# Kernel optimization log

Measured on AMD Instinct MI355X. Metric: run time of the kernel, lower is better.

Reference implementation:

```python
import jax, jax.numpy as jnp
import numpy as np

B, S, IN_DIM, D, H, L = 2, 2048, 64, 512, 8, 2
DK = D // H
EPS = 1e-5

def _layernorm(x, g, b):
    mu = jnp.mean(x, axis=-1, keepdims=True)
    var = jnp.mean((x - mu) ** 2, axis=-1, keepdims=True)
    return (x - mu) * jax.lax.rsqrt(var + EPS) * g + b

def _prob_sparse_layer(x, Wq, bq, Wk, bk, Wv, bv, fcW, fcb, ln_g, ln_b):
    # x: [B, S, D]
    Bs, Ss, _ = x.shape
    Q = (x @ Wq + bq).reshape(Bs, Ss, H, DK).transpose(0, 2, 1, 3)  # [B,H,S,DK]
    K = (x @ Wk + bk).reshape(Bs, Ss, H, DK).transpose(0, 2, 1, 3)
    V = (x @ Wv + bv).reshape(Bs, Ss, H, DK).transpose(0, 2, 1, 3)
    scores = jnp.einsum('bhqd,bhkd->bhqk', Q, K) / np.sqrt(DK).astype(np.float32)
    k = max(1, Ss // 10)
    top_scores, _ = jax.lax.top_k(scores, k)          # [B,H,S,k]
    threshold = top_scores[..., -1:]                  # k-th largest per row
    sparse_scores = jnp.where(scores < threshold, -jnp.inf, scores)
    attn = jax.nn.softmax(sparse_scores, axis=-1)     # dropout is identity in eval
    out = jnp.einsum('bhqk,bhkd->bhqd', attn, V)
    out = out.transpose(0, 2, 1, 3).reshape(Bs, Ss, D)
    out = out @ fcW + fcb
    return _layernorm(x + out, ln_g, ln_b)

def setup_inputs() -> dict:
    key = jax.random.key(0)
    ks = jax.random.split(key, 16)
    sd = 1.0 / np.sqrt(D)
    sdi = 1.0 / np.sqrt(IN_DIM)
    return {
        'x': jax.random.normal(ks[0], (B, S, IN_DIM), jnp.float32),
        'enc_W': jax.random.normal(ks[1], (IN_DIM, D), jnp.float32) * sdi,
        'enc_b': jnp.zeros((D,), jnp.float32),
        'Wq': jax.random.normal(ks[2], (L, D, D), jnp.float32) * sd,
        'bq': jnp.zeros((L, D), jnp.float32),
        'Wk': jax.random.normal(ks[3], (L, D, D), jnp.float32) * sd,
        'bk': jnp.zeros((L, D), jnp.float32),
        'Wv': jax.random.normal(ks[4], (L, D, D), jnp.float32) * sd,
        'bv': jnp.zeros((L, D), jnp.float32),
        'fcW': jax.random.normal(ks[5], (L, D, D), jnp.float32) * sd,
        'fcb': jnp.zeros((L, D), jnp.float32),
        'ln_g': jnp.ones((L, D), jnp.float32),
        'ln_b': jnp.zeros((L, D), jnp.float32),
        'dec_W': jax.random.normal(ks[6], (D, IN_DIM), jnp.float32) * sd,
        'dec_b': jnp.zeros((IN_DIM,), jnp.float32),
    }

def reference(x, enc_W, enc_b, Wq, bq, Wk, bk, Wv, bv, fcW, fcb, ln_g, ln_b, dec_W, dec_b):
    h = x @ enc_W + enc_b  # [B,S,D]
    for i in range(Wq.shape[0]):
        h = _prob_sparse_layer(h, Wq[i], bq[i], Wk[i], bk[i], Wv[i], bv[i],
                               fcW[i], fcb[i], ln_g[i], ln_b[i])
    return h[:, -1, :] @ dec_W + dec_b  # [B, IN_DIM]
```

## Files before the change

kernel.cpp:

```cpp
#include <hip/hip_runtime.h>
#include <hip/hip_bf16.h>

typedef unsigned short u16;
typedef __bf16 bf16x8 __attribute__((ext_vector_type(8)));
typedef u16 u16x8 __attribute__((ext_vector_type(8)));
typedef float f32x4 __attribute__((ext_vector_type(4)));

#define S_LEN 2048
#define NH 8
#define DMODEL 512
#define TOPK 204

__device__ __forceinline__ u16 f2b(float f) {
  __hip_bfloat16 h = __float2bfloat16(f);
  return __builtin_bit_cast(u16, h);
}
__device__ __forceinline__ unsigned f2b_fast(float f) {
  unsigned u = __float_as_uint(f);
  return (u + 0x7FFFu + ((u >> 16) & 1u)) >> 16;
}
__device__ __forceinline__ float kunmap(unsigned k) {
  unsigned tb = (k & 0x8000u) ? (k ^ 0x8000u) : (~k & 0xFFFFu);
  return __uint_as_float(tb << 16);
}
__device__ __forceinline__ unsigned fkmap(float f) {
  unsigned b = __float_as_uint(f) >> 16;
  return b ^ ((b & 0x8000u) ? 0xFFFFu : 0x8000u);
}

__global__ void transpose_w(const float* __restrict__ in, u16* __restrict__ out, int R, int C) {
  __shared__ float tile[32][33];
  int c0 = blockIdx.x * 32, r0 = blockIdx.y * 32;
  int tx = threadIdx.x & 31, ty = threadIdx.x >> 5;
#pragma unroll
  for (int i = 0; i < 32; i += 8)
    tile[ty + i][tx] = in[(long long)(r0 + ty + i) * C + c0 + tx];
  __syncthreads();
#pragma unroll
  for (int i = 0; i < 32; i += 8)
    out[(long long)(c0 + ty + i) * R + r0 + tx] = f2b(tile[tx][ty + i]);
}

__global__ void transpose_w4(const float* __restrict__ W0, const float* __restrict__ W1,
                             const float* __restrict__ W2, const float* __restrict__ W3,
                             u16* __restrict__ O0, u16* __restrict__ O1,
                             u16* __restrict__ O2, u16* __restrict__ O3) {
  __shared__ float tile[32][33];
  const float* in;
  u16* out;
  switch (blockIdx.z) {
    case 0: in = W0; out = O0; break;
    case 1: in = W1; out = O1; break;
    case 2: in = W2; out = O2; break;
    default: in = W3; out = O3; break;
  }
  int c0 = blockIdx.x * 32, r0 = blockIdx.y * 32;
  int tx = threadIdx.x & 31, ty = threadIdx.x >> 5;
#pragma unroll
  for (int i = 0; i < 32; i += 8)
    tile[ty + i][tx] = in[(long long)(r0 + ty + i) * 512 + c0 + tx];
  __syncthreads();
#pragma unroll
  for (int i = 0; i < 32; i += 8)
    out[(long long)(c0 + ty + i) * 512 + r0 + tx] = f2b(tile[tx][ty + i]);
}

__global__ void conv_b(const float* __restrict__ in, u16* __restrict__ out, int n) {
  int i = blockIdx.x * 256 + threadIdx.x;
  if (i < n) out[i] = f2b(in[i]);
}

template <int MODE>
__global__ __launch_bounds__(256) void gemm_bt(
    const u16* __restrict__ A, const u16* __restrict__ BT,
    const float* __restrict__ bias, const float* __restrict__ biasK, const float* __restrict__ biasV,
    float* __restrict__ outF, u16* __restrict__ outB, u16* __restrict__ outBK, u16* __restrict__ outBV,
    int M, int N, int K, float scale) {
  __shared__ u16 As[64 * 32];
  __shared__ u16 Bs[128 * 32];
  int n0 = blockIdx.x * 128, m0 = blockIdx.y * 64;
  int t = threadIdx.x;
  int lane = t & 63, wv = t >> 6;
  int mw = (wv & 1) * 32, nw = (wv >> 1) * 64;
  int fr = lane & 15, fg = lane >> 4;
  f32x4 acc[2][4] = {};
  for (int kt = 0; kt < K; kt += 32) {
    int e0 = t * 8;
    int r0r = e0 >> 5, c0c = e0 & 31;
    int e1 = e0 + 2048;
    int r1r = e1 >> 5, c1c = e1 & 31;
    *(u16x8*)&As[e0] = *(const u16x8*)&A[(long long)(m0 + r0r) * K + kt + c0c];
    *(u16x8*)&Bs[e0] = *(const u16x8*)&BT[(long long)(n0 + r0r) * K + kt + c0c];
    *(u16x8*)&Bs[e1] = *(const u16x8*)&BT[(long long)(n0 + r1r) * K + kt + c1c];
    __syncthreads();
    bf16x8 af[2], bfv[4];
#pragma unroll
    for (int i = 0; i < 2; i++) af[i] = *(const bf16x8*)&As[(mw + i * 16 + fr) * 32 + fg * 8];
#pragma unroll
    for (int j = 0; j < 4; j++) bfv[j] = *(const bf16x8*)&Bs[(nw + j * 16 + fr) * 32 + fg * 8];
#pragma unroll
    for (int i = 0; i < 2; i++)
#pragma unroll
      for (int j = 0; j < 4; j++)
        acc[i][j] = __builtin_amdgcn_mfma_f32_16x16x32_bf16(af[i], bfv[j], acc[i][j], 0, 0, 0);
    __syncthreads();
  }
#pragma unroll
  for (int i = 0; i < 2; i++)
#pragma unroll
    for (int j = 0; j < 4; j++) {
      int mloc = mw + i * 16 + fg * 4;
      int n = n0 + nw + j * 16 + fr;
      float bvl;
      if constexpr (MODE == 5) {
        int seg = n >> 9, nn = n & 511;
        bvl = (seg == 0 ? bias : seg == 1 ? biasK : biasV)[nn];
      } else {
        bvl = bias ? bias[n] : 0.f;
      }
#pragma unroll
      for (int r = 0; r < 4; r++) {
        int m = m0 + mloc + r;
        float v = acc[i][j][r] * scale + bvl;
        if constexpr (MODE == 0) {
          outF[(long long)m * N + n] = v;
        } else if constexpr (MODE == 4) {
          outF[(long long)m * N + n] = v;
          outB[(long long)m * N + n] = f2b(v);
        } else if constexpr (MODE == 5) {
          int seg = n >> 9, nn = n & 511;
          if (seg == 0) v *= 0.125f;
          u16 val = f2b(v);
          if (seg == 2) {
            outBV[((long long)((m >> 11) * NH + (nn >> 6)) * 64 + (nn & 63)) * S_LEN + (m & 2047)] = val;
          } else {
            long long qkidx = (long long)((m >> 11) * NH + (nn >> 6)) * (S_LEN * 64) +
                              (long long)(m & 2047) * 64 + (nn & 63);
            if (seg == 0) outB[qkidx] = val;
            else outBK[qkidx] = val;
          }
        }
      }
    }
}

__global__ __launch_bounds__(1024, 8) void score_pv(
    const u16* __restrict__ Qb, const u16* __restrict__ Kb, const u16* __restrict__ VTb,
    u16* __restrict__ aoB) {
  __shared__ u16 Qs[16 * 64];
  __shared__ __align__(16) u16 Ss[16 * 2048];
  __shared__ float thrS[16];
  __shared__ float mS[16];
  __shared__ float zS[16 * 16];
  int flat = blockIdx.x;
  int xcd = flat & 7, local = flat >> 3;
  int bh = xcd * 2 + (local >> 7);
  int m0 = (local & 127) * 16;
  int t = threadIdx.x;
  int lane = t & 63, wv = t >> 6, fr = lane & 15, fg = lane >> 4;
  const u16* Qg = Qb + ((long long)bh * S_LEN + m0) * 64;
  const u16* Kg = Kb + (long long)bh * S_LEN * 64;
  const u16* Vg = VTb + (long long)bh * 64 * S_LEN;
  if (t < 128) {
    int row = t >> 3, cc = t & 7;
    *(u16x8*)&Qs[row * 64 + ((cc ^ (row & 7)) * 8)] = *(const u16x8*)&Qg[row * 64 + cc * 8];
  }
  __syncthreads();
  bf16x8 aq[2];
#pragma unroll
  for (int ks = 0; ks < 2; ks++)
    aq[ks] = *(const bf16x8*)&Qs[fr * 64 + (((fg + 4 * ks) ^ (fr & 7)) * 8)];

#pragma unroll 4
  for (int tt = 0; tt < 8; tt++) {
    int col0 = wv * 128 + tt * 16;
    f32x4 acc = {};
#pragma unroll
    for (int ks = 0; ks < 2; ks++) {
      bf16x8 bk = *(const bf16x8*)&Kg[(long long)(col0 + fr) * 64 + ks * 32 + fg * 8];
      acc = __builtin_amdgcn_mfma_f32_16x16x32_bf16(bk, aq[ks], acc, 0, 0, 0);
    }
    uint2 w;
    w.x = f2b_fast(acc[0]) | (f2b_fast(acc[1]) << 16);
    w.y = f2b_fast(acc[2]) | (f2b_fast(acc[3]) << 16);
    int row = fr, col = col0 + fg * 4;
    *(uint2*)&Ss[row * 2048 + (col ^ ((row & 15) << 3))] = w;
  }
  __syncthreads();

  {
    int rr = wv;
    const uint2* cu2 = (const uint2*)&Ss[rr * 2048];
    float kf[32];
#pragma unroll
    for (int j = 0; j < 8; j++) {
      uint2 w = cu2[lane + 64 * j];
      kf[4 * j + 0] = __uint_as_float(w.x << 16);
      kf[4 * j + 1] = __uint_as_float(w.x & 0xFFFF0000u);
      kf[4 * j + 2] = __uint_as_float(w.y << 16);
      kf[4 * j + 3] = __uint_as_float(w.y & 0xFFFF0000u);
    }
    float mxf = kf[0];
#pragma unroll
    for (int j = 1; j < 32; j++) mxf = fmaxf(mxf, kf[j]);
#pragma unroll
    for (int o = 1; o < 64; o <<= 1)
      mxf = fmaxf(mxf, __uint_as_float((unsigned)__shfl_xor((int)__float_as_uint(mxf), o)));
    unsigned mxi = fkmap(mxf);
    unsigned lo, hi;
    unsigned lo0 = mxi > 384u ? mxi - 384u : 0u;
    {
      float pf = kunmap(lo0);
      int c = 0;
#pragma unroll
      for (int j = 0; j < 32; j++) c += (int)__popcll(__ballot(kf[j] >= pf));
      if (c >= TOPK) { lo = lo0; hi = mxi; }
      else { lo = 0u; hi = lo0 - 1u; }
    }
    while (lo < hi) {
      unsigned mid = (lo + hi + 1u) >> 1;
      float midf = kunmap(mid);
      int c = 0;
#pragma unroll
      for (int j = 0; j < 32; j++) c += (int)__popcll(__ballot(kf[j] >= midf));
      if (c >= TOPK) lo = mid; else hi = mid - 1u;
    }
    if (lane == 0) {
      thrS[rr] = kunmap(lo);
      mS[rr] = mxf;
    }
  }
  __syncthreads();

  float thrF = thrS[fr];
  float myM = mS[fr];
  float zpart = 0.f;
  f32x4 acc_o[4] = {};
#pragma unroll 2
  for (int step = 0; step < 4; step++) {
    int k0 = wv * 128 + step * 32;
    u16x8 kk = *(const u16x8*)&Ss[fr * 2048 + ((k0 + fg * 8) ^ ((fr & 15) << 3))];
    unsigned wp[4];
#pragma unroll
    for (int e2 = 0; e2 < 4; e2++) {
      float s0 = __uint_as_float((unsigned)kk[2 * e2] << 16);
      float s1 = __uint_as_float((unsigned)kk[2 * e2 + 1] << 16);
      float p0 = (s0 >= thrF) ? __expf(s0 - myM) : 0.f;
      float p1 = (s1 >= thrF) ? __expf(s1 - myM) : 0.f;
      zpart += p0 + p1;
      wp[e2] = f2b_fast(p0) | (f2b_fast(p1) << 16);
    }
    bf16x8 pa = *(bf16x8*)&wp;
#pragma unroll
    for (int j = 0; j < 4; j++) {
      bf16x8 bv = *(const bf16x8*)&Vg[(long long)(j * 16 + fr) * 2048 + k0 + fg * 8];
      acc_o[j] = __builtin_amdgcn_mfma_f32_16x16x32_bf16(pa, bv, acc_o[j], 0, 0, 0);
    }
  }
  zpart += __shfl_xor(zpart, 16);
  zpart += __shfl_xor(zpart, 32);
  __syncthreads();

  float* Of = (float*)Ss;
#pragma unroll
  for (int j = 0; j < 4; j++)
#pragma unroll
    for (int r = 0; r < 4; r++) {
      int row = fg * 4 + r, col = j * 16 + fr;
      Of[wv * 1024 + row * 64 + (col ^ ((row >> 2) << 3))] = acc_o[j][r];
    }
  if (fg == 0) zS[wv * 16 + fr] = zpart;
  __syncthreads();
  long long ob = (long long)(bh >> 3) * S_LEN * DMODEL + (bh & 7) * 64;
  {
    int row = t >> 6, dk = t & 63;
    int sw = dk ^ ((row >> 2) << 3);
    float s = 0.f;
#pragma unroll
    for (int w = 0; w < 16; w++) s += Of[w * 1024 + row * 64 + sw];
    float z = 0.f;
#pragma unroll
    for (int w = 0; w < 16; w++) z += zS[w * 16 + row];
    aoB[ob + (long long)(m0 + row) * DMODEL + dk] = f2b(s / z);
  }
}

__global__ __launch_bounds__(256) void resid_ln(const float* __restrict__ h, const float* __restrict__ fco,
                                                const float* __restrict__ g, const float* __restrict__ b,
                                                float* __restrict__ hout, u16* __restrict__ hbout) {
  __shared__ float red[4];
  int row = blockIdx.x;
  int t = threadIdx.x;
  long long base = (long long)row * 512;
  float v0 = h[base + t] + fco[base + t];
  float v1 = h[base + t + 256] + fco[base + t + 256];
  float s = v0 + v1;
#pragma unroll
  for (int o = 32; o > 0; o >>= 1) s += __shfl_down(s, o);
  if ((t & 63) == 0) red[t >> 6] = s;
  __syncthreads();
  float mu = (red[0] + red[1] + red[2] + red[3]) * (1.f / 512.f);
  float d0 = v0 - mu, d1 = v1 - mu;
  float q = d0 * d0 + d1 * d1;
#pragma unroll
  for (int o = 32; o > 0; o >>= 1) q += __shfl_down(q, o);
  __syncthreads();
  if ((t & 63) == 0) red[t >> 6] = q;
  __syncthreads();
  float var = (red[0] + red[1] + red[2] + red[3]) * (1.f / 512.f);
  float rs = rsqrtf(var + 1e-5f);
  float y0 = d0 * rs * g[t] + b[t];
  float y1 = d1 * rs * g[t + 256] + b[t + 256];
  hout[base + t] = y0;
  hout[base + t + 256] = y1;
  hbout[base + t] = f2b(y0);
  hbout[base + t + 256] = f2b(y1);
}

__global__ void decoder_k(const float* __restrict__ h, const float* __restrict__ W,
                          const float* __restrict__ bias, float* __restrict__ out) {
  int t = threadIdx.x;
  int b = t >> 6, j = t & 63;
  const float* hr = h + ((long long)b * S_LEN + (S_LEN - 1)) * DMODEL;
  float s = 0.f;
  for (int d = 0; d < DMODEL; d++) s += hr[d] * W[(long long)d * 64 + j];
  out[t] = s + bias[j];
}

extern "C" void kernel_launch(void* const* d_in, const int* in_sizes, int n_in,
                              void* d_out, int out_size, void* d_ws, size_t ws_size,
                              hipStream_t stream) {
  const float* x = (const float*)d_in[0];
  const float* enc_W = (const float*)d_in[1];
  const float* enc_b = (const float*)d_in[2];
  const float* Wq = (const float*)d_in[3];
  const float* bq = (const float*)d_in[4];
  const float* Wk = (const float*)d_in[5];
  const float* bk = (const float*)d_in[6];
  const float* Wv = (const float*)d_in[7];
  const float* bv = (const float*)d_in[8];
  const float* fcW = (const float*)d_in[9];
  const float* fcb = (const float*)d_in[10];
  const float* ln_g = (const float*)d_in[11];
  const float* ln_b = (const float*)d_in[12];
  const float* dec_W = (const float*)d_in[13];
  const float* dec_b = (const float*)d_in[14];

  char* p = (char*)d_ws;
  auto alloc = [&](size_t bytes) {
    char* r = p;
    p += (bytes + 255) & ~(size_t)255;
    return r;
  };
  const size_t BS = 2 * (size_t)S_LEN;
  u16* encWT = (u16*)alloc(512 * 64 * 2);
  u16* xbf = (u16*)alloc(BS * 64 * 2);
  float* hF = (float*)alloc(BS * 512 * 4);
  u16* hB = (u16*)alloc(BS * 512 * 2);
  u16* WqT = (u16*)alloc(512 * 512 * 2);
  u16* WkT = (u16*)alloc(512 * 512 * 2);
  u16* WvT = (u16*)alloc(512 * 512 * 2);
  u16* fcWT = (u16*)alloc(512 * 512 * 2);
  u16* Qb = (u16*)alloc((size_t)16 * 2048 * 64 * 2);
  u16* Kb = (u16*)alloc((size_t)16 * 2048 * 64 * 2);
  u16* VTb = (u16*)alloc((size_t)16 * 2048 * 64 * 2);
  u16* aoB = (u16*)alloc(BS * 512 * 2);
  float* fcO = (float*)Qb;

  transpose_w<<<dim3(16, 2), 256, 0, stream>>>(enc_W, encWT, 64, 512);
  conv_b<<<(int)(BS * 64 / 256), 256, 0, stream>>>(x, xbf, (int)(BS * 64));
  gemm_bt<4><<<dim3(4, 64), 256, 0, stream>>>(xbf, encWT, enc_b, nullptr, nullptr,
                                              hF, hB, nullptr, nullptr, 4096, 512, 64, 1.f);

  for (int l = 0; l < 2; l++) {
    transpose_w4<<<dim3(16, 16, 4), 256, 0, stream>>>(
        Wq + (size_t)l * 512 * 512, Wk + (size_t)l * 512 * 512,
        Wv + (size_t)l * 512 * 512, fcW + (size_t)l * 512 * 512,
        WqT, WkT, WvT, fcWT);
    gemm_bt<5><<<dim3(12, 64), 256, 0, stream>>>(hB, WqT, bq + l * 512, bk + l * 512, bv + l * 512,
                                                 nullptr, Qb, Kb, VTb, 4096, 1536, 512, 1.f);
    score_pv<<<dim3(2048), 1024, 0, stream>>>(Qb, Kb, VTb, aoB);
    gemm_bt<0><<<dim3(4, 64), 256, 0, stream>>>(aoB, fcWT, fcb + l * 512, nullptr, nullptr,
                                                fcO, nullptr, nullptr, nullptr, 4096, 512, 512, 1.f);
    resid_ln<<<4096, 256, 0, stream>>>(hF, fcO, ln_g + l * 512, ln_b + l * 512, hF, hB);
  }
  decoder_k<<<1, 128, 0, stream>>>(hF, dec_W, dec_b, (float*)d_out);
}
```

Measured before the change: 391.9 us.

## Fuse row max into score pass, prefetch K/V, vectorize reductions, split decoder

Computes the per-row score maximum during the QK^T MFMA pass via shuffles and an LDS atomicMax, removing a separate max reduction before the top-k threshold search. K and V fragments are software-prefetched one iteration ahead, and bf16 conversions are replaced with truncation. The output reduction is rewritten to use vectorized f32x4 LDS stores and loads with a precomputed reciprocal normalizer. The decoder is parallelized across more threads and blocks. Truncation slightly changes rounding of scores and probabilities, and the lower occupancy hint may affect register allocation.

```diff
diff --git a/kernel.cpp b/kernel.cpp
--- a/kernel.cpp
+++ b/kernel.cpp
@@ -15,15 +15,11 @@
   __hip_bfloat16 h = __float2bfloat16(f);
   return __builtin_bit_cast(u16, h);
 }
-__device__ __forceinline__ unsigned f2b_fast(float f) {
-  unsigned u = __float_as_uint(f);
-  return (u + 0x7FFFu + ((u >> 16) & 1u)) >> 16;
-}
 __device__ __forceinline__ float kunmap(unsigned k) {
   unsigned tb = (k & 0x8000u) ? (k ^ 0x8000u) : (~k & 0xFFFFu);
   return __uint_as_float(tb << 16);
 }
-__device__ __forceinline__ unsigned fkmap(float f) {
+__device__ __forceinline__ unsigned fkmap_t(float f) {
   unsigned b = __float_as_uint(f) >> 16;
   return b ^ ((b & 0x8000u) ? 0xFFFFu : 0x8000u);
 }
@@ -144,14 +140,16 @@
     }
 }
 
-__global__ __launch_bounds__(1024, 8) void score_pv(
+__global__ __launch_bounds__(1024, 4) void score_pv(
     const u16* __restrict__ Qb, const u16* __restrict__ Kb, const u16* __restrict__ VTb,
     u16* __restrict__ aoB) {
   __shared__ u16 Qs[16 * 64];
   __shared__ __align__(16) u16 Ss[16 * 2048];
+  __shared__ unsigned maxkS[16];
   __shared__ float thrS[16];
   __shared__ float mS[16];
   __shared__ float zS[16 * 16];
+  __shared__ float rzS[16];
   int flat = blockIdx.x;
   int xcd = flat & 7, local = flat >> 3;
   int bh = xcd * 2 + (local >> 7);
@@ -161,6 +159,7 @@
   const u16* Qg = Qb + ((long long)bh * S_LEN + m0) * 64;
   const u16* Kg = Kb + (long long)bh * S_LEN * 64;
   const u16* Vg = VTb + (long long)bh * 64 * S_LEN;
+  if (t < 16) maxkS[t] = 0u;
   if (t < 128) {
     int row = t >> 3, cc = t & 7;
     *(u16x8*)&Qs[row * 64 + ((cc ^ (row & 7)) * 8)] = *(const u16x8*)&Qg[row * 64 + cc * 8];
@@ -171,51 +170,65 @@
   for (int ks = 0; ks < 2; ks++)
     aq[ks] = *(const bf16x8*)&Qs[fr * 64 + (((fg + 4 * ks) ^ (fr & 7)) * 8)];
 
-#pragma unroll 4
+  float rowmax = -3e38f;
+  int colb = wv * 128;
+  bf16x8 ka = *(const bf16x8*)&Kg[(long long)(colb + fr) * 64 + fg * 8];
+  bf16x8 kb = *(const bf16x8*)&Kg[(long long)(colb + fr) * 64 + 32 + fg * 8];
+#pragma unroll
   for (int tt = 0; tt < 8; tt++) {
-    int col0 = wv * 128 + tt * 16;
+    bf16x8 na = ka, nb = kb;
+    if (tt < 7) {
+      int c2 = colb + (tt + 1) * 16;
+      na = *(const bf16x8*)&Kg[(long long)(c2 + fr) * 64 + fg * 8];
+      nb = *(const bf16x8*)&Kg[(long long)(c2 + fr) * 64 + 32 + fg * 8];
+    }
     f32x4 acc = {};
-#pragma unroll
-    for (int ks = 0; ks < 2; ks++) {
-      bf16x8 bk = *(const bf16x8*)&Kg[(long long)(col0 + fr) * 64 + ks * 32 + fg * 8];
-      acc = __builtin_amdgcn_mfma_f32_16x16x32_bf16(bk, aq[ks], acc, 0, 0, 0);
-    }
+    acc = __builtin_amdgcn_mfma_f32_16x16x32_bf16(ka, aq[0], acc, 0, 0, 0);
+    acc = __builtin_amdgcn_mfma_f32_16x16x32_bf16(kb, aq[1], acc, 0, 0, 0);
+    rowmax = fmaxf(fmaxf(acc[0], acc[1]), fmaxf(rowmax, fmaxf(acc[2], acc[3])));
+    unsigned u0 = __float_as_uint(acc[0]), u1 = __float_as_uint(acc[1]);
+    unsigned u2 = __float_as_uint(acc[2]), u3 = __float_as_uint(acc[3]);
     uint2 w;
-    w.x = f2b_fast(acc[0]) | (f2b_fast(acc[1]) << 16);
-    w.y = f2b_fast(acc[2]) | (f2b_fast(acc[3]) << 16);
-    int row = fr, col = col0 + fg * 4;
-    *(uint2*)&Ss[row * 2048 + (col ^ ((row & 15) << 3))] = w;
-  }
+    w.x = (u0 >> 16) | (u1 & 0xFFFF0000u);
+    w.y = (u2 >> 16) | (u3 & 0xFFFF0000u);
+    int col = colb + tt * 16 + fg * 4;
+    *(uint2*)&Ss[fr * 2048 + (col ^ ((fr & 15) << 3))] = w;
+    ka = na;
+    kb = nb;
+  }
+  rowmax = fmaxf(rowmax, __uint_as_float((unsigned)__shfl_xor((int)__float_as_uint(rowmax), 16)));
+  rowmax = fmaxf(rowmax, __uint_as_float((unsigned)__shfl_xor((int)__float_as_uint(rowmax), 32)));
+  if (fg == 0) atomicMax(&maxkS[fr], fkmap_t(rowmax));
   __syncthreads();
 
   {
     int rr = wv;
-    const uint2* cu2 = (const uint2*)&Ss[rr * 2048];
+    unsigned mxi = __builtin_amdgcn_readfirstlane(maxkS[rr]);
+    unsigned swz = (unsigned)((rr & 15) << 3);
     float kf[32];
 #pragma unroll
-    for (int j = 0; j < 8; j++) {
-      uint2 w = cu2[lane + 64 * j];
-      kf[4 * j + 0] = __uint_as_float(w.x << 16);
-      kf[4 * j + 1] = __uint_as_float(w.x & 0xFFFF0000u);
-      kf[4 * j + 2] = __uint_as_float(w.y << 16);
-      kf[4 * j + 3] = __uint_as_float(w.y & 0xFFFF0000u);
-    }
-    float mxf = kf[0];
-#pragma unroll
-    for (int j = 1; j < 32; j++) mxf = fmaxf(mxf, kf[j]);
-#pragma unroll
-    for (int o = 1; o < 64; o <<= 1)
-      mxf = fmaxf(mxf, __uint_as_float((unsigned)__shfl_xor((int)__float_as_uint(mxf), o)));
-    unsigned mxi = fkmap(mxf);
+    for (int j2 = 0; j2 < 4; j2++) {
+      uint4 q = *(const uint4*)&Ss[rr * 2048 + (((unsigned)(lane * 8 + j2 * 512)) ^ swz)];
+      kf[8 * j2 + 0] = __uint_as_float(q.x << 16);
+      kf[8 * j2 + 1] = __uint_as_float(q.x & 0xFFFF0000u);
+      kf[8 * j2 + 2] = __uint_as_float(q.y << 16);
+      kf[8 * j2 + 3] = __uint_as_float(q.y & 0xFFFF0000u);
+      kf[8 * j2 + 4] = __uint_as_float(q.z << 16);
+      kf[8 * j2 + 5] = __uint_as_float(q.z & 0xFFFF0000u);
+      kf[8 * j2 + 6] = __uint_as_float(q.w << 16);
+      kf[8 * j2 + 7] = __uint_as_float(q.w & 0xFFFF0000u);
+    }
     unsigned lo, hi;
-    unsigned lo0 = mxi > 384u ? mxi - 384u : 0u;
-    {
+    if (mxi > 384u) {
+      unsigned lo0 = mxi - 384u;
       float pf = kunmap(lo0);
       int c = 0;
 #pragma unroll
       for (int j = 0; j < 32; j++) c += (int)__popcll(__ballot(kf[j] >= pf));
       if (c >= TOPK) { lo = lo0; hi = mxi; }
       else { lo = 0u; hi = lo0 - 1u; }
+    } else {
+      lo = 0u; hi = mxi;
     }
     while (lo < hi) {
       unsigned mid = (lo + hi + 1u) >> 1;
@@ -227,7 +240,7 @@
     }
     if (lane == 0) {
       thrS[rr] = kunmap(lo);
-      mS[rr] = mxf;
+      mS[rr] = kunmap(mxi);
     }
   }
   __syncthreads();
@@ -236,10 +249,23 @@
   float myM = mS[fr];
   float zpart = 0.f;
   f32x4 acc_o[4] = {};
-#pragma unroll 2
+  int kbase = wv * 128;
+  bf16x8 bv0 = *(const bf16x8*)&Vg[(long long)(0 * 16 + fr) * 2048 + kbase + fg * 8];
+  bf16x8 bv1 = *(const bf16x8*)&Vg[(long long)(1 * 16 + fr) * 2048 + kbase + fg * 8];
+  bf16x8 bv2 = *(const bf16x8*)&Vg[(long long)(2 * 16 + fr) * 2048 + kbase + fg * 8];
+  bf16x8 bv3 = *(const bf16x8*)&Vg[(long long)(3 * 16 + fr) * 2048 + kbase + fg * 8];
+#pragma unroll
   for (int step = 0; step < 4; step++) {
-    int k0 = wv * 128 + step * 32;
-    u16x8 kk = *(const u16x8*)&Ss[fr * 2048 + ((k0 + fg * 8) ^ ((fr & 15) << 3))];
+    int kc = kbase + step * 32;
+    bf16x8 n0 = bv0, n1 = bv1, n2 = bv2, n3 = bv3;
+    if (step < 3) {
+      int kn = kc + 32;
+      n0 = *(const bf16x8*)&Vg[(long long)(0 * 16 + fr) * 2048 + kn + fg * 8];
+      n1 = *(const bf16x8*)&Vg[(long long)(1 * 16 + fr) * 2048 + kn + fg * 8];
+      n2 = *(const bf16x8*)&Vg[(long long)(2 * 16 + fr) * 2048 + kn + fg * 8];
+      n3 = *(const bf16x8*)&Vg[(long long)(3 * 16 + fr) * 2048 + kn + fg * 8];
+    }
+    u16x8 kk = *(const u16x8*)&Ss[fr * 2048 + ((kc + fg * 8) ^ ((fr & 15) << 3))];
     unsigned wp[4];
 #pragma unroll
     for (int e2 = 0; e2 < 4; e2++) {
@@ -248,14 +274,14 @@
       float p0 = (s0 >= thrF) ? __expf(s0 - myM) : 0.f;
       float p1 = (s1 >= thrF) ? __expf(s1 - myM) : 0.f;
       zpart += p0 + p1;
-      wp[e2] = f2b_fast(p0) | (f2b_fast(p1) << 16);
+      wp[e2] = (__float_as_uint(p0) >> 16) | (__float_as_uint(p1) & 0xFFFF0000u);
     }
     bf16x8 pa = *(bf16x8*)&wp;
-#pragma unroll
-    for (int j = 0; j < 4; j++) {
-      bf16x8 bv = *(const bf16x8*)&Vg[(long long)(j * 16 + fr) * 2048 + k0 + fg * 8];
-      acc_o[j] = __builtin_amdgcn_mfma_f32_16x16x32_bf16(pa, bv, acc_o[j], 0, 0, 0);
-    }
+    acc_o[0] = __builtin_amdgcn_mfma_f32_16x16x32_bf16(pa, bv0, acc_o[0], 0, 0, 0);
+    acc_o[1] = __builtin_amdgcn_mfma_f32_16x16x32_bf16(pa, bv1, acc_o[1], 0, 0, 0);
+    acc_o[2] = __builtin_amdgcn_mfma_f32_16x16x32_bf16(pa, bv2, acc_o[2], 0, 0, 0);
+    acc_o[3] = __builtin_amdgcn_mfma_f32_16x16x32_bf16(pa, bv3, acc_o[3], 0, 0, 0);
+    bv0 = n0; bv1 = n1; bv2 = n2; bv3 = n3;
   }
   zpart += __shfl_xor(zpart, 16);
   zpart += __shfl_xor(zpart, 32);
@@ -263,25 +289,34 @@
 
   float* Of = (float*)Ss;
 #pragma unroll
-  for (int j = 0; j < 4; j++)
-#pragma unroll
-    for (int r = 0; r < 4; r++) {
-      int row = fg * 4 + r, col = j * 16 + fr;
-      Of[wv * 1024 + row * 64 + (col ^ ((row >> 2) << 3))] = acc_o[j][r];
-    }
+  for (int j = 0; j < 4; j++) {
+    int col = j * 16 + fr;
+    int grp = col * 4 + (fg ^ (col & 3));
+    *(f32x4*)&Of[wv * 1024 + grp * 4] = acc_o[j];
+  }
   if (fg == 0) zS[wv * 16 + fr] = zpart;
   __syncthreads();
-  long long ob = (long long)(bh >> 3) * S_LEN * DMODEL + (bh & 7) * 64;
-  {
-    int row = t >> 6, dk = t & 63;
-    int sw = dk ^ ((row >> 2) << 3);
-    float s = 0.f;
-#pragma unroll
-    for (int w = 0; w < 16; w++) s += Of[w * 1024 + row * 64 + sw];
+  if (t < 16) {
     float z = 0.f;
 #pragma unroll
-    for (int w = 0; w < 16; w++) z += zS[w * 16 + row];
-    aoB[ob + (long long)(m0 + row) * DMODEL + dk] = f2b(s / z);
+    for (int w = 0; w < 16; w++) z += zS[w * 16 + t];
+    rzS[t] = 1.0f / z;
+  }
+  __syncthreads();
+  if (t < 256) {
+    int col = t & 63, rowq = t >> 6;
+    f32x4 s = {};
+#pragma unroll
+    for (int w = 0; w < 16; w++) {
+      int grp = col * 4 + (rowq ^ (col & 3));
+      f32x4 v = *(const f32x4*)&Of[w * 1024 + grp * 4];
+      s += v;
+    }
+    f32x4 rz = *(const f32x4*)&rzS[rowq * 4];
+    long long ob = (long long)(bh >> 3) * S_LEN * DMODEL + (bh & 7) * 64;
+#pragma unroll
+    for (int r = 0; r < 4; r++)
+      aoB[ob + (long long)(m0 + rowq * 4 + r) * DMODEL + col] = f2b(s[r] * rz[r]);
   }
 }
 
@@ -317,14 +352,24 @@
   hbout[base + t + 256] = f2b(y1);
 }
 
-__global__ void decoder_k(const float* __restrict__ h, const float* __restrict__ W,
-                          const float* __restrict__ bias, float* __restrict__ out) {
+__global__ __launch_bounds__(512) void decoder_k(const float* __restrict__ h, const float* __restrict__ W,
+                                                 const float* __restrict__ bias, float* __restrict__ out) {
+  __shared__ float part[8][64];
+  int b = blockIdx.x;
   int t = threadIdx.x;
-  int b = t >> 6, j = t & 63;
+  int j = t & 63, ds = t >> 6;
   const float* hr = h + ((long long)b * S_LEN + (S_LEN - 1)) * DMODEL;
   float s = 0.f;
-  for (int d = 0; d < DMODEL; d++) s += hr[d] * W[(long long)d * 64 + j];
-  out[t] = s + bias[j];
+#pragma unroll 8
+  for (int d = ds * 64; d < ds * 64 + 64; d++) s += hr[d] * W[(long long)d * 64 + j];
+  part[ds][j] = s;
+  __syncthreads();
+  if (t < 64) {
+    float acc = part[0][t];
+#pragma unroll
+    for (int w = 1; w < 8; w++) acc += part[w][t];
+    out[b * 64 + t] = acc + bias[t];
+  }
 }
 
 extern "C" void kernel_launch(void* const* d_in, const int* in_sizes, int n_in,
@@ -384,5 +429,5 @@
                                                 fcO, nullptr, nullptr, nullptr, 4096, 512, 512, 1.f);
     resid_ln<<<4096, 256, 0, stream>>>(hF, fcO, ln_g + l * 512, ln_b + l * 512, hF, hB);
   }
-  decoder_k<<<1, 128, 0, stream>>>(hF, dec_W, dec_b, (float*)d_out);
-}
+  decoder_k<<<2, 512, 0, stream>>>(hF, dec_W, dec_b, (float*)d_out);
+}
```

After: 482.0 us. +23.0%, slower.
